# Performance work log

Hardware: AMD Instinct MI355X
Metric: run time of the kernel (lower is better)

## Reference

```python
import jax, jax.numpy as jnp
import numpy as np

B = 64          # batch == number of parallel fc layers used
T = 512         # sequence length
IN_FEATS = 1024
OUT_FEATS = 1024


def setup_inputs() -> dict:
    key = jax.random.key(0)
    kx, kw, kb = jax.random.split(key, 3)
    x = jax.random.normal(kx, (B, T, IN_FEATS), dtype=jnp.float32)
    # Per-sample Linear weights, stacked: W[i] is the weight of list_fc[i]
    # (torch Linear weight layout: [out_feats, in_feats])
    bound = 1.0 / np.sqrt(IN_FEATS)
    W = jax.random.uniform(kw, (B, OUT_FEATS, IN_FEATS), dtype=jnp.float32,
                           minval=-bound, maxval=bound)
    b = jax.random.uniform(kb, (B, OUT_FEATS), dtype=jnp.float32,
                           minval=-bound, maxval=bound)
    return {"x": x, "W": W, "b": b}


def reference(x, W, b):
    # Equivalent to: cat([list_fc[i](x[i:i+1]) for i in range(B)], dim=0)
    # i.e. a grouped GEMM with group size 1: out[i] = x[i] @ W[i].T + b[i]
    out = jnp.einsum('bti,boi->bto', x, W)  # [B, T, OUT]
    return out + b[:, None, :]
```

## Files before the change

kernel.cpp:

```cpp
#include <hip/hip_runtime.h>
#include <hip/hip_bf16.h>

#define BATCH 64
#define MDIM 512
#define NDIM 1024
#define KDIM 1024

#define BM 256
#define BN 256
#define BK 64
#define NKT (KDIM / BK)

typedef __attribute__((ext_vector_type(4))) float f32x4;
typedef __attribute__((ext_vector_type(8))) short bf16x8;
typedef __attribute__((ext_vector_type(4))) unsigned int u32x4;

__device__ __forceinline__ unsigned int cvt2(float lo, float hi) {
    __hip_bfloat162 h = __float22bfloat162_rn(float2{lo, hi});
    return *(unsigned int*)&h;
}

#define MFMA16(a, b, c) __builtin_amdgcn_mfma_f32_16x16x32_bf16((a), (b), (c), 0, 0, 0)
#define SB0 __builtin_amdgcn_sched_barrier(0)
#define WAITLG(n) do { asm volatile("s_waitcnt lgkmcnt(" #n ")" ::: "memory"); SB0; } while (0)
#define BAR do { SB0; __builtin_amdgcn_s_barrier(); SB0; } while (0)

__global__ __launch_bounds__(512, 2)
void grouped_fc_kernel(const float* __restrict__ X,
                       const float* __restrict__ W,
                       const float* __restrict__ Bias,
                       float* __restrict__ Out) {
    const int swz  = (blockIdx.x & 7) * 64 + (blockIdx.x >> 3);
    const int bidx = swz >> 3;
    const int tile = swz & 7;
    const int tm = tile & 1;
    const int tn = tile >> 1;

    const int tid  = threadIdx.x;
    const int lane = tid & 63;
    const int wid  = tid >> 6;
    const int wm   = wid & 1;
    const int wn   = wid >> 1;

    __shared__ unsigned short ldsA[2][BM][BK];
    __shared__ unsigned short ldsB[2][BN][BK];

    const float* srcA = X + ((size_t)bidx * MDIM + (size_t)tm * BM) * KDIM;
    const float* srcB = W + ((size_t)bidx * NDIM + (size_t)tn * BN) * KDIM;

    const int s_r  = tid >> 2;
    const int s_cf = (tid & 3) * 16;
    const int s_x  = s_r & 7;
    const int so0  = (((tid & 3) * 2)     ^ s_x) * 8;
    const int so1  = (((tid & 3) * 2 + 1) ^ s_x) * 8;

    f32x4 st0[4], st1[4];

    auto ISSUE = [&](const float* srcbase, int hv, int kt_, f32x4 (&s)[4]) {
        const float* p = srcbase + (size_t)(hv * 128 + s_r) * KDIM + kt_ * BK + s_cf;
#pragma unroll
        for (int v = 0; v < 4; ++v) s[v] = *(const f32x4*)(p + v * 4);
    };

    auto CVTW = [&](unsigned short* ldsbase, int hv, f32x4 (&s)[4]) {
        const int row = hv * 128 + s_r;
        u32x4 w0, w1;
        w0[0] = cvt2(s[0][0], s[0][1]); w0[1] = cvt2(s[0][2], s[0][3]);
        w0[2] = cvt2(s[1][0], s[1][1]); w0[3] = cvt2(s[1][2], s[1][3]);
        w1[0] = cvt2(s[2][0], s[2][1]); w1[1] = cvt2(s[2][2], s[2][3]);
        w1[2] = cvt2(s[3][0], s[3][1]); w1[3] = cvt2(s[3][2], s[3][3]);
        *(u32x4*)&ldsbase[(size_t)row * BK + so0] = w0;
        *(u32x4*)&ldsbase[(size_t)row * BK + so1] = w1;
    };

    const int frow = lane & 15;
    const int khi  = lane >> 4;
    const int xr   = frow & 7;
    const int oK0  = ((khi)     ^ xr) * 8;
    const int oK1  = ((4 + khi) ^ xr) * 8;

    auto rdA = [&](int buf, int mi, int o) {
        return *(const bf16x8*)&ldsA[buf][wm * 128 + mi * 16 + frow][o];
    };
    auto rdB = [&](int buf, int ni, int o) {
        return *(const bf16x8*)&ldsB[buf][wn * 64 + ni * 16 + frow][o];
    };

    f32x4 acc[8][4];
#pragma unroll
    for (int mi = 0; mi < 8; ++mi)
#pragma unroll
        for (int ni = 0; ni < 4; ++ni)
            acc[mi][ni] = (f32x4){0.f, 0.f, 0.f, 0.f};

    ISSUE(srcA, 0, 0, st0); ISSUE(srcA, 1, 0, st1);
    CVTW(&ldsA[0][0][0], 0, st0); CVTW(&ldsA[0][0][0], 1, st1);
    ISSUE(srcB, 0, 0, st0); ISSUE(srcB, 1, 0, st1);
    CVTW(&ldsB[0][0][0], 0, st0); CVTW(&ldsB[0][0][0], 1, st1);
    ISSUE(srcA, 0, 1, st0); ISSUE(srcA, 1, 1, st1);
    WAITLG(0);
    BAR;

    bf16x8 af[8], bfr[4];

#pragma unroll 1
    for (int kt = 0; kt < NKT - 1; ++kt) {
        const int rd = kt & 1;
        const bool m2 = (kt + 2 < NKT);
        unsigned short* nA = &ldsA[rd ^ 1][0][0];
        unsigned short* nB = &ldsB[rd ^ 1][0][0];

#pragma unroll
        for (int mi = 0; mi < 8; ++mi) af[mi] = rdA(rd, mi, oK0);
        bfr[0] = rdB(rd, 0, oK0); bfr[1] = rdB(rd, 1, oK0);
        WAITLG(0);
        __builtin_amdgcn_s_setprio(1);
#pragma unroll
        for (int mi = 0; mi < 8; ++mi) {
            acc[mi][0] = MFMA16(af[mi], bfr[0], acc[mi][0]);
            acc[mi][1] = MFMA16(af[mi], bfr[1], acc[mi][1]);
        }
        __builtin_amdgcn_s_setprio(0);
        SB0;
        bfr[2] = rdB(rd, 2, oK0); bfr[3] = rdB(rd, 3, oK0);
        CVTW(nA, 0, st0);
        ISSUE(srcB, 0, kt + 1, st0);
        BAR;

        WAITLG(2);
        __builtin_amdgcn_s_setprio(1);
#pragma unroll
        for (int mi = 0; mi < 8; ++mi) {
            acc[mi][2] = MFMA16(af[mi], bfr[2], acc[mi][2]);
            acc[mi][3] = MFMA16(af[mi], bfr[3], acc[mi][3]);
        }
        __builtin_amdgcn_s_setprio(0);
        SB0;
#pragma unroll
        for (int mi = 0; mi < 8; ++mi) af[mi] = rdA(rd, mi, oK1);
        bfr[0] = rdB(rd, 0, oK1); bfr[1] = rdB(rd, 1, oK1);
        CVTW(nA, 1, st1);
        ISSUE(srcB, 1, kt + 1, st1);
        BAR;

        WAITLG(2);
        __builtin_amdgcn_s_setprio(1);
#pragma unroll
        for (int mi = 0; mi < 8; ++mi) {
            acc[mi][0] = MFMA16(af[mi], bfr[0], acc[mi][0]);
            acc[mi][1] = MFMA16(af[mi], bfr[1], acc[mi][1]);
        }
        __builtin_amdgcn_s_setprio(0);
        SB0;
        bfr[2] = rdB(rd, 2, oK1); bfr[3] = rdB(rd, 3, oK1);
        CVTW(nB, 0, st0);
        if (m2) ISSUE(srcA, 0, kt + 2, st0);
        BAR;

        WAITLG(2);
        __builtin_amdgcn_s_setprio(1);
#pragma unroll
        for (int mi = 0; mi < 8; ++mi) {
            acc[mi][2] = MFMA16(af[mi], bfr[2], acc[mi][2]);
            acc[mi][3] = MFMA16(af[mi], bfr[3], acc[mi][3]);
        }
        __builtin_amdgcn_s_setprio(0);
        SB0;
        CVTW(nB, 1, st1);
        if (m2) ISSUE(srcA, 1, kt + 2, st1);
        WAITLG(0);
        BAR;
    }

    {
        const int rd = (NKT - 1) & 1;
#pragma unroll
        for (int mi = 0; mi < 8; ++mi) af[mi] = rdA(rd, mi, oK0);
#pragma unroll
        for (int ni = 0; ni < 4; ++ni) bfr[ni] = rdB(rd, ni, oK0);
        WAITLG(0);
#pragma unroll
        for (int mi = 0; mi < 8; ++mi)
#pragma unroll
            for (int ni = 0; ni < 4; ++ni)
                acc[mi][ni] = MFMA16(af[mi], bfr[ni], acc[mi][ni]);
#pragma unroll
        for (int mi = 0; mi < 8; ++mi) af[mi] = rdA(rd, mi, oK1);
#pragma unroll
        for (int ni = 0; ni < 4; ++ni) bfr[ni] = rdB(rd, ni, oK1);
        WAITLG(0);
#pragma unroll
        for (int mi = 0; mi < 8; ++mi)
#pragma unroll
            for (int ni = 0; ni < 4; ++ni)
                acc[mi][ni] = MFMA16(af[mi], bfr[ni], acc[mi][ni]);
    }

#pragma unroll
    for (int ni = 0; ni < 4; ++ni) {
        const int gc = tn * BN + wn * 64 + ni * 16 + frow;
        const float bv = Bias[bidx * NDIM + gc];
#pragma unroll
        for (int mi = 0; mi < 8; ++mi) {
            const int gr0 = tm * BM + wm * 128 + mi * 16 + khi * 4;
            float* po = Out + ((size_t)bidx * MDIM + gr0) * NDIM + gc;
#pragma unroll
            for (int r = 0; r < 4; ++r)
                po[(size_t)r * NDIM] = acc[mi][ni][r] + bv;
        }
    }
}

extern "C" void kernel_launch(void* const* d_in, const int* in_sizes, int n_in,
                              void* d_out, int out_size, void* d_ws, size_t ws_size,
                              hipStream_t stream) {
    const float* X  = (const float*)d_in[0];
    const float* W  = (const float*)d_in[1];
    const float* Bs = (const float*)d_in[2];
    float* Out = (float*)d_out;

    grouped_fc_kernel<<<dim3(512), dim3(512), 0, stream>>>(X, W, Bs, Out);
}
```

Baseline: 138.5 us.

## Restructure K-loop to prefetch all A/B tiles at once with single barrier

Replaces the four-phase K-loop, which staggered A and B global loads across phases with a barrier after each, by a two-phase loop. Each iteration now issues every global load for the next K tile at the top, runs two full 8x4 MFMA blocks, and converts and writes to LDS before a single barrier. This cuts barriers per iteration from four to one and gives global loads a whole iteration of MFMA work to hide behind. In exchange it doubles staging registers (four f32x4[4] arrays), which may raise register pressure at launch_bounds(512,2), and it changes the wait-count ordering of LDS traffic.

```diff
diff --git a/kernel.cpp b/kernel.cpp
--- a/kernel.cpp
+++ b/kernel.cpp
@@ -54,9 +54,9 @@
     const int so0  = (((tid & 3) * 2)     ^ s_x) * 8;
     const int so1  = (((tid & 3) * 2 + 1) ^ s_x) * 8;
 
-    f32x4 st0[4], st1[4];
+    f32x4 sa0[4], sa1[4], sb0[4], sb1[4];
 
-    auto ISSUE = [&](const float* srcbase, int hv, int kt_, f32x4 (&s)[4]) {
+    auto ISSUE1 = [&](const float* srcbase, int hv, int kt_, f32x4 (&s)[4]) {
         const float* p = srcbase + (size_t)(hv * 128 + s_r) * KDIM + kt_ * BK + s_cf;
 #pragma unroll
         for (int v = 0; v < 4; ++v) s[v] = *(const f32x4*)(p + v * 4);
@@ -93,11 +93,10 @@
         for (int ni = 0; ni < 4; ++ni)
             acc[mi][ni] = (f32x4){0.f, 0.f, 0.f, 0.f};
 
-    ISSUE(srcA, 0, 0, st0); ISSUE(srcA, 1, 0, st1);
-    CVTW(&ldsA[0][0][0], 0, st0); CVTW(&ldsA[0][0][0], 1, st1);
-    ISSUE(srcB, 0, 0, st0); ISSUE(srcB, 1, 0, st1);
-    CVTW(&ldsB[0][0][0], 0, st0); CVTW(&ldsB[0][0][0], 1, st1);
-    ISSUE(srcA, 0, 1, st0); ISSUE(srcA, 1, 1, st1);
+    ISSUE1(srcA, 0, 0, sa0); ISSUE1(srcA, 1, 0, sa1);
+    ISSUE1(srcB, 0, 0, sb0); ISSUE1(srcB, 1, 0, sb1);
+    CVTW(&ldsA[0][0][0], 0, sa0); CVTW(&ldsA[0][0][0], 1, sa1);
+    CVTW(&ldsB[0][0][0], 0, sb0); CVTW(&ldsB[0][0][0], 1, sb1);
     WAITLG(0);
     BAR;
 
@@ -106,68 +105,44 @@
 #pragma unroll 1
     for (int kt = 0; kt < NKT - 1; ++kt) {
         const int rd = kt & 1;
-        const bool m2 = (kt + 2 < NKT);
         unsigned short* nA = &ldsA[rd ^ 1][0][0];
         unsigned short* nB = &ldsB[rd ^ 1][0][0];
 
+        ISSUE1(srcA, 0, kt + 1, sa0); ISSUE1(srcA, 1, kt + 1, sa1);
+        ISSUE1(srcB, 0, kt + 1, sb0); ISSUE1(srcB, 1, kt + 1, sb1);
+        SB0;
+
 #pragma unroll
         for (int mi = 0; mi < 8; ++mi) af[mi] = rdA(rd, mi, oK0);
-        bfr[0] = rdB(rd, 0, oK0); bfr[1] = rdB(rd, 1, oK0);
+#pragma unroll
+        for (int ni = 0; ni < 4; ++ni) bfr[ni] = rdB(rd, ni, oK0);
         WAITLG(0);
         __builtin_amdgcn_s_setprio(1);
 #pragma unroll
-        for (int mi = 0; mi < 8; ++mi) {
-            acc[mi][0] = MFMA16(af[mi], bfr[0], acc[mi][0]);
-            acc[mi][1] = MFMA16(af[mi], bfr[1], acc[mi][1]);
-        }
+        for (int mi = 0; mi < 8; ++mi)
+#pragma unroll
+            for (int ni = 0; ni < 4; ++ni)
+                acc[mi][ni] = MFMA16(af[mi], bfr[ni], acc[mi][ni]);
         __builtin_amdgcn_s_setprio(0);
         SB0;
-        bfr[2] = rdB(rd, 2, oK0); bfr[3] = rdB(rd, 3, oK0);
-        CVTW(nA, 0, st0);
-        ISSUE(srcB, 0, kt + 1, st0);
-        BAR;
 
-        WAITLG(2);
+#pragma unroll
+        for (int mi = 0; mi < 8; ++mi) af[mi] = rdA(rd, mi, oK1);
+#pragma unroll
+        for (int ni = 0; ni < 4; ++ni) bfr[ni] = rdB(rd, ni, oK1);
+        SB0;
+        CVTW(nA, 0, sa0); CVTW(nA, 1, sa1);
+        WAITLG(4);
         __builtin_amdgcn_s_setprio(1);
 #pragma unroll
-        for (int mi = 0; mi < 8; ++mi) {
-            acc[mi][2] = MFMA16(af[mi], bfr[2], acc[mi][2]);
-            acc[mi][3] = MFMA16(af[mi], bfr[3], acc[mi][3]);
-        }
+        for (int mi = 0; mi < 8; ++mi)
+#pragma unroll
+            for (int ni = 0; ni < 4; ++ni)
+                acc[mi][ni] = MFMA16(af[mi], bfr[ni], acc[mi][ni]);
         __builtin_amdgcn_s_setprio(0);
         SB0;
-#pragma unroll
-        for (int mi = 0; mi < 8; ++mi) af[mi] = rdA(rd, mi, oK1);
-        bfr[0] = rdB(rd, 0, oK1); bfr[1] = rdB(rd, 1, oK1);
-        CVTW(nA, 1, st1);
-        ISSUE(srcB, 1, kt + 1, st1);
-        BAR;
 
-        WAITLG(2);
-        __builtin_amdgcn_s_setprio(1);
-#pragma unroll
-        for (int mi = 0; mi < 8; ++mi) {
-            acc[mi][0] = MFMA16(af[mi], bfr[0], acc[mi][0]);
-            acc[mi][1] = MFMA16(af[mi], bfr[1], acc[mi][1]);
-        }
-        __builtin_amdgcn_s_setprio(0);
-        SB0;
-        bfr[2] = rdB(rd, 2, oK1); bfr[3] = rdB(rd, 3, oK1);
-        CVTW(nB, 0, st0);
-        if (m2) ISSUE(srcA, 0, kt + 2, st0);
-        BAR;
-
-        WAITLG(2);
-        __builtin_amdgcn_s_setprio(1);
-#pragma unroll
-        for (int mi = 0; mi < 8; ++mi) {
-            acc[mi][2] = MFMA16(af[mi], bfr[2], acc[mi][2]);
-            acc[mi][3] = MFMA16(af[mi], bfr[3], acc[mi][3]);
-        }
-        __builtin_amdgcn_s_setprio(0);
-        SB0;
-        CVTW(nB, 1, st1);
-        if (m2) ISSUE(srcA, 1, kt + 2, st1);
+        CVTW(nB, 0, sb0); CVTW(nB, 1, sb1);
         WAITLG(0);
         BAR;
     }
```

Measured after the change: 161.2 us. 1.16x slower.
